# Kernel tuning notes

Measured on AMD Instinct MI355X. Metric: run time of the kernel, lower is better.

Reference implementation:

```python
import jax, jax.numpy as jnp
import numpy as np

EPS = 1e-5

def _ln(x, g, b):
    mu = jnp.mean(x, axis=-1, keepdims=True)
    var = jnp.mean((x - mu) ** 2, axis=-1, keepdims=True)
    return (x - mu) / jnp.sqrt(var + EPS) * g + b

def setup_inputs() -> dict:
    key = jax.random.key(0)
    ks = jax.random.split(key, 8)
    S, B, L, M, D, Nq, H = 4, 256, 256, 4, 512, 4, 2048
    G = (M + 2) * D
    inp = {
        'ns_tokens': jax.random.normal(ks[0], (B, M, D), jnp.float32),
        'seq_tokens': jax.random.normal(ks[1], (S, B, L, D), jnp.float32),
        'seq_padding_masks': jax.random.randint(ks[2], (S, B, L), 0, 2).astype(bool),
        'seq_stats': jax.random.normal(ks[3], (S, B, 6), jnp.float32),
        'gin_gamma': jnp.ones((G,), jnp.float32),
        'gin_beta': jnp.zeros((G,), jnp.float32),
        'stat_W': 0.02 * jax.random.normal(ks[4], (S, 6, D), jnp.float32),
        'stat_b': jnp.zeros((S, D), jnp.float32),
        'stat_ln_g': jnp.ones((S, D), jnp.float32),
        'stat_ln_b': jnp.zeros((S, D), jnp.float32),
        'W1': 0.02 * jax.random.normal(ks[5], (S, Nq, G, H), jnp.float32),
        'b1': jnp.zeros((S, Nq, H), jnp.float32),
        'W2': 0.02 * jax.random.normal(ks[6], (S, Nq, H, D), jnp.float32),
        'b2': jnp.zeros((S, Nq, D), jnp.float32),
        'ln_g': jnp.ones((S, Nq, D), jnp.float32),
        'ln_b': jnp.zeros((S, Nq, D), jnp.float32),
    }
    return inp

def reference(ns_tokens, seq_tokens, seq_padding_masks, seq_stats,
              gin_gamma, gin_beta, stat_W, stat_b, stat_ln_g, stat_ln_b,
              W1, b1, W2, b2, ln_g, ln_b):
    S, B = seq_tokens.shape[0], ns_tokens.shape[0]
    ns_flat = ns_tokens.reshape(B, -1)                       # (B, M*D)
    valid = (~seq_padding_masks).astype(seq_tokens.dtype)[..., None]  # (S,B,L,1)
    denom = jnp.clip(jnp.sum(valid, axis=2), 1.0)            # (S,B,1)
    pooled = jnp.sum(seq_tokens * valid, axis=2) / denom     # (S,B,D)
    stat = jnp.einsum('sbf,sfd->sbd', seq_stats, stat_W) + stat_b[:, None]
    stat = _ln(stat, stat_ln_g[:, None], stat_ln_b[:, None])  # (S,B,D)
    gi = jnp.concatenate([jnp.broadcast_to(ns_flat[None], (S, B, ns_flat.shape[1])), pooled, stat], axis=-1)
    gi = _ln(gi, gin_gamma, gin_beta)                        # (S,B,G)
    h = jax.nn.silu(jnp.einsum('sbg,sqgh->sqbh', gi, W1) + b1[:, :, None])
    q = jnp.einsum('sqbh,sqhd->sqbd', h, W2) + b2[:, :, None]
    q = _ln(q, ln_g[:, :, None], ln_b[:, :, None])           # (S,Nq,B,D)
    return jnp.transpose(q, (0, 2, 1, 3))                    # (S,B,Nq,D)
```

## Files before the change

kernel.cpp:

```cpp
#include <hip/hip_runtime.h>
#include <hip/hip_bf16.h>

#define S_ 4
#define B_ 256
#define L_ 256
#define D_ 512
#define NQ_ 4
#define H_ 2048
#define G_ 3072

typedef __attribute__((ext_vector_type(4))) float f32x4;
typedef __attribute__((ext_vector_type(8))) short s16x8;

__device__ __forceinline__ unsigned short f2bf(float x) {
    __hip_bfloat16 hb = __float2bfloat16(x);
    return reinterpret_cast<unsigned short&>(hb);
}

__device__ __forceinline__ void gll16(const void* g, void* l) {
    __builtin_amdgcn_global_load_lds(
        (const __attribute__((address_space(1))) unsigned int*)g,
        (__attribute__((address_space(3))) unsigned int*)l, 16, 0, 0);
}

__device__ __forceinline__ float block_sum256(float v, float* red) {
    #pragma unroll
    for (int off = 32; off > 0; off >>= 1) v += __shfl_down(v, off, 64);
    int tid = threadIdx.x;
    int lane = tid & 63, wid = tid >> 6;
    if (lane == 0) red[wid] = v;
    __syncthreads();
    float r = (tid < 4) ? red[tid] : 0.f;
    #pragma unroll
    for (int off = 4; off > 0; off >>= 1) r += __shfl_down(r, off, 64);
    if (tid == 0) red[0] = r;
    __syncthreads();
    float out = red[0];
    __syncthreads();
    return out;
}

__global__ __launch_bounds__(256) void poolgi_kernel(
    const float* __restrict__ seq_tokens,
    const unsigned char* __restrict__ masks_raw,
    const float* __restrict__ ns_tokens,
    const float* __restrict__ seq_stats,
    const float* __restrict__ stat_W,
    const float* __restrict__ stat_b,
    const float* __restrict__ stat_ln_g,
    const float* __restrict__ stat_ln_b,
    const float* __restrict__ gin_gamma,
    const float* __restrict__ gin_beta,
    __hip_bfloat16* __restrict__ gi)
{
    const int sb = blockIdx.x;
    const int s = sb >> 8;
    const int b = sb & 255;
    const int tid = threadIdx.x;

    __shared__ float sval[L_];
    __shared__ float scount[4];
    __shared__ f32x4 spart[256];
    __shared__ float spool[D_];
    __shared__ float sstat[D_];
    __shared__ float red[8];
    __shared__ int is_bool_flag;

    if (tid == 0) is_bool_flag = 0;
    __syncthreads();
    {
        unsigned int w = reinterpret_cast<const unsigned int*>(masks_raw)[tid];
        if (w & 0xFFFFFF00u) is_bool_flag = 1;
    }
    __syncthreads();
    const bool is_bool = (is_bool_flag != 0);

    int mval;
    if (is_bool) mval = masks_raw[(size_t)sb * L_ + tid];
    else         mval = reinterpret_cast<const int*>(masks_raw)[(size_t)sb * L_ + tid];
    float valid = mval ? 0.f : 1.f;
    sval[tid] = valid;
    float c = valid;
    #pragma unroll
    for (int off = 32; off > 0; off >>= 1) c += __shfl_down(c, off, 64);
    if ((tid & 63) == 0) scount[tid >> 6] = c;
    __syncthreads();
    const float denom = fmaxf(scount[0] + scount[1] + scount[2] + scount[3], 1.f);

    const float* base = seq_tokens + (size_t)sb * L_ * D_;
    const int cidx = tid & 127;
    const int rg = tid >> 7;
    f32x4 acc = {0.f, 0.f, 0.f, 0.f};
    for (int l = rg; l < L_; l += 2) {
        float vl = sval[l];
        f32x4 v = *reinterpret_cast<const f32x4*>(base + (size_t)l * D_ + cidx * 4);
        acc += v * vl;
    }
    spart[tid] = acc;
    __syncthreads();
    if (tid < 128) {
        f32x4 r = spart[tid] + spart[tid + 128];
        r *= (1.f / denom);
        *reinterpret_cast<f32x4*>(&spool[cidx * 4]) = r;
    }
    __syncthreads();

    float st[6];
    #pragma unroll
    for (int f = 0; f < 6; ++f) st[f] = seq_stats[(size_t)sb * 6 + f];

    float sp[2];
    #pragma unroll
    for (int k = 0; k < 2; ++k) {
        int d = tid + k * 256;
        float a = stat_b[s * D_ + d];
        #pragma unroll
        for (int f = 0; f < 6; ++f) a += st[f] * stat_W[(s * 6 + f) * D_ + d];
        sp[k] = a;
    }
    float ssum = block_sum256(sp[0] + sp[1], red);
    float ssq  = block_sum256(sp[0] * sp[0] + sp[1] * sp[1], red);
    float mu = ssum / D_;
    float var = ssq / D_ - mu * mu;
    float rinv = rsqrtf(var + 1e-5f);
    #pragma unroll
    for (int k = 0; k < 2; ++k) {
        int d = tid + k * 256;
        sstat[d] = (sp[k] - mu) * rinv * stat_ln_g[s * D_ + d] + stat_ln_b[s * D_ + d];
    }
    __syncthreads();

    float gv[12];
    float gsum = 0.f, gsq = 0.f;
    #pragma unroll
    for (int k = 0; k < 12; ++k) {
        int g = tid + k * 256;
        float v;
        if (g < 2048)       v = ns_tokens[(size_t)b * 2048 + g];
        else if (g < 2560)  v = spool[g - 2048];
        else                v = sstat[g - 2560];
        gv[k] = v;
        gsum += v;
        gsq += v * v;
    }
    gsum = block_sum256(gsum, red);
    gsq  = block_sum256(gsq, red);
    mu = gsum / G_;
    var = gsq / G_ - mu * mu;
    rinv = rsqrtf(var + 1e-5f);
    #pragma unroll
    for (int k = 0; k < 12; ++k) {
        int g = tid + k * 256;
        float o = (gv[k] - mu) * rinv * gin_gamma[g] + gin_beta[g];
        gi[(size_t)sb * G_ + g] = __float2bfloat16(o);
    }
}

__global__ __launch_bounds__(256) void gemm1_kernel(
    const __hip_bfloat16* __restrict__ gi,
    const float* __restrict__ W1,
    const float* __restrict__ b1,
    __hip_bfloat16* __restrict__ hbuf)
{
    const int bid = blockIdx.x;
    const int wg = (bid & 7) * 64 + (bid >> 3);
    const int ntile = wg & 31;
    const int sq = wg >> 5;
    const int s = sq >> 2;
    const int tid = threadIdx.x;
    const int lane = tid & 63;
    const int wid = tid >> 6;

    __shared__ __align__(16) unsigned short As[2][256 * 64];
    __shared__ __align__(16) unsigned short Ws[2][64 * 64];

    const __hip_bfloat16* Ab = gi + (size_t)s * B_ * G_;
    const float* Wb = W1 + (size_t)sq * G_ * H_ + ntile * 64;

    f32x4 acc[4][4];
    #pragma unroll
    for (int i = 0; i < 4; ++i)
        #pragma unroll
        for (int j = 0; j < 4; ++j) acc[i][j] = (f32x4){0.f, 0.f, 0.f, 0.f};

    const __hip_bfloat16* aptr[8];
    #pragma unroll
    for (int i = 0; i < 8; ++i) {
        int row = wid * 64 + i * 8 + (lane >> 3);
        int swz = ((lane >> 3) ^ i) & 7;
        aptr[i] = Ab + (size_t)row * G_ + (((lane & 7) ^ swz) * 8);
    }

    const int wn0 = (tid & 15) * 4;
    const int wk0 = (tid >> 4) * 4;
    int offW[4];
    #pragma unroll
    for (int nn = 0; nn < 4; ++nn) {
        int row = wn0 + nn;
        int swz = (row ^ (row >> 3)) & 7;
        offW[nn] = (row * 128 + wk0 * 2) ^ (swz << 4);
    }

    int offA[2][4], offB[2][4];
    #pragma unroll
    for (int kb = 0; kb < 2; ++kb) {
        #pragma unroll
        for (int mi = 0; mi < 4; ++mi) {
            int r = wid * 64 + mi * 16 + (lane & 15);
            int swz = (r ^ (r >> 3)) & 7;
            offA[kb][mi] = r * 128 + ((((lane >> 4) + kb * 4) ^ swz) * 16);
        }
        #pragma unroll
        for (int ni = 0; ni < 4; ++ni) {
            int r = ni * 16 + (lane & 15);
            int swz = (r ^ (r >> 3)) & 7;
            offB[kb][ni] = r * 128 + ((((lane >> 4) + kb * 4) ^ swz) * 16);
        }
    }

    {
        #pragma unroll
        for (int i = 0; i < 8; ++i)
            gll16(aptr[i], &As[0][(wid * 64 + i * 8) * 64]);
        const float* wp = Wb + (size_t)wk0 * H_ + wn0;
        f32x4 w0[4];
        #pragma unroll
        for (int kk = 0; kk < 4; ++kk)
            w0[kk] = *reinterpret_cast<const f32x4*>(wp + (size_t)kk * H_);
        #pragma unroll
        for (int nn = 0; nn < 4; ++nn) {
            unsigned long long pk =
                (unsigned long long)f2bf(w0[0][nn]) |
                ((unsigned long long)f2bf(w0[1][nn]) << 16) |
                ((unsigned long long)f2bf(w0[2][nn]) << 32) |
                ((unsigned long long)f2bf(w0[3][nn]) << 48);
            *reinterpret_cast<unsigned long long*>(reinterpret_cast<char*>(&Ws[0][0]) + offW[nn]) = pk;
        }
        __syncthreads();
    }

    for (int kt = 0; kt < G_ / 64; ++kt) {
        const int cur = kt & 1, nxt = cur ^ 1;
        const bool pf = (kt < G_ / 64 - 1);
        f32x4 wv[4];
        if (pf) {
            const int kb2 = (kt + 1) * 64;
            #pragma unroll
            for (int i = 0; i < 8; ++i)
                gll16(aptr[i] + kb2, &As[nxt][(wid * 64 + i * 8) * 64]);
            const float* wp = Wb + (size_t)(kb2 + wk0) * H_ + wn0;
            #pragma unroll
            for (int kk = 0; kk < 4; ++kk)
                wv[kk] = *reinterpret_cast<const f32x4*>(wp + (size_t)kk * H_);
        }

        const char* Al = reinterpret_cast<const char*>(&As[cur][0]);
        const char* Wl = reinterpret_cast<const char*>(&Ws[cur][0]);
        #pragma unroll
        for (int kb = 0; kb < 2; ++kb) {
            s16x8 af[4], bfr[4];
            #pragma unroll
            for (int mi = 0; mi < 4; ++mi)
                af[mi] = *reinterpret_cast<const s16x8*>(Al + offA[kb][mi]);
            #pragma unroll
            for (int ni = 0; ni < 4; ++ni)
                bfr[ni] = *reinterpret_cast<const s16x8*>(Wl + offB[kb][ni]);
            #pragma unroll
            for (int mi = 0; mi < 4; ++mi)
                #pragma unroll
                for (int ni = 0; ni < 4; ++ni)
                    acc[mi][ni] = __builtin_amdgcn_mfma_f32_16x16x32_bf16(af[mi], bfr[ni], acc[mi][ni], 0, 0, 0);
        }

        if (pf) {
            #pragma unroll
            for (int nn = 0; nn < 4; ++nn) {
                unsigned long long pk =
                    (unsigned long long)f2bf(wv[0][nn]) |
                    ((unsigned long long)f2bf(wv[1][nn]) << 16) |
                    ((unsigned long long)f2bf(wv[2][nn]) << 32) |
                    ((unsigned long long)f2bf(wv[3][nn]) << 48);
                *reinterpret_cast<unsigned long long*>(reinterpret_cast<char*>(&Ws[nxt][0]) + offW[nn]) = pk;
            }
        }
        __syncthreads();
    }

    const float* b1p = b1 + (size_t)sq * H_ + ntile * 64;
    __hip_bfloat16* hp = hbuf + (size_t)sq * B_ * H_;
    #pragma unroll
    for (int mi = 0; mi < 4; ++mi)
        #pragma unroll
        for (int ni = 0; ni < 4; ++ni)
            #pragma unroll
            for (int r = 0; r < 4; ++r) {
                int row = wid * 64 + mi * 16 + ((lane >> 4) << 2) + r;
                int coll = ni * 16 + (lane & 15);
                float x = acc[mi][ni][r] + b1p[coll];
                float sg = 1.f / (1.f + __expf(-x));
                hp[(size_t)row * H_ + ntile * 64 + coll] = __float2bfloat16(x * sg);
            }
}

__global__ __launch_bounds__(256) void gemm2_kernel(
    const __hip_bfloat16* __restrict__ hbuf,
    const float* __restrict__ W2,
    float* __restrict__ qpre)
{
    const int ntile = blockIdx.x;
    const int mtile = blockIdx.y;
    const int sq = blockIdx.z;
    const int tid = threadIdx.x;
    const int lane = tid & 63;
    const int wid = tid >> 6;
    const int wm = wid >> 1, wn = wid & 1;

    __shared__ __align__(16) unsigned short As[128 * 64];
    __shared__ __align__(16) unsigned short Ws[64 * 64];

    const __hip_bfloat16* Ab = hbuf + ((size_t)sq * B_ + mtile * 128) * H_;
    const float* Wb = W2 + (size_t)sq * H_ * D_ + ntile * 64;

    f32x4 acc[4][2];
    #pragma unroll
    for (int i = 0; i < 4; ++i)
        #pragma unroll
        for (int j = 0; j < 2; ++j) acc[i][j] = (f32x4){0.f, 0.f, 0.f, 0.f};

    const int wn0 = (tid & 15) * 4;
    const int wk0 = (tid >> 4) * 4;

    for (int kt = 0; kt < H_ / 64; ++kt) {
        const int kbase = kt * 64;
        __syncthreads();
        #pragma unroll
        for (int i = 0; i < 4; ++i) {
            int slot = i * 256 + tid;
            int row = slot >> 3, cc = slot & 7;
            int swz = (row ^ (row >> 3)) & 7;
            s16x8 v = *reinterpret_cast<const s16x8*>(Ab + (size_t)row * H_ + kbase + cc * 8);
            *reinterpret_cast<s16x8*>(&As[row * 64 + ((cc ^ swz) * 8)]) = v;
        }
        float wv[4][4];
        #pragma unroll
        for (int kk = 0; kk < 4; ++kk) {
            f32x4 t = *reinterpret_cast<const f32x4*>(Wb + (size_t)(kbase + wk0 + kk) * D_ + wn0);
            #pragma unroll
            for (int j = 0; j < 4; ++j) wv[kk][j] = t[j];
        }
        #pragma unroll
        for (int nn = 0; nn < 4; ++nn) {
            int row = wn0 + nn;
            int swz = (row ^ (row >> 3)) & 7;
            unsigned long long pk =
                (unsigned long long)f2bf(wv[0][nn]) |
                ((unsigned long long)f2bf(wv[1][nn]) << 16) |
                ((unsigned long long)f2bf(wv[2][nn]) << 32) |
                ((unsigned long long)f2bf(wv[3][nn]) << 48);
            int byteoff = (row * 128 + wk0 * 2) ^ (swz << 4);
            *reinterpret_cast<unsigned long long*>(reinterpret_cast<char*>(Ws) + byteoff) = pk;
        }
        __syncthreads();
        #pragma unroll
        for (int kb = 0; kb < 2; ++kb) {
            s16x8 af[4], bfr[2];
            #pragma unroll
            for (int mi = 0; mi < 4; ++mi) {
                int r = wm * 64 + mi * 16 + (lane & 15);
                int swz = (r ^ (r >> 3)) & 7;
                int chunk = ((lane >> 4) + kb * 4) ^ swz;
                af[mi] = *reinterpret_cast<const s16x8*>(&As[r * 64 + chunk * 8]);
            }
            #pragma unroll
            for (int ni = 0; ni < 2; ++ni) {
                int r = wn * 32 + ni * 16 + (lane & 15);
                int swz = (r ^ (r >> 3)) & 7;
                int chunk = ((lane >> 4) + kb * 4) ^ swz;
                bfr[ni] = *reinterpret_cast<const s16x8*>(&Ws[r * 64 + chunk * 8]);
            }
            #pragma unroll
            for (int mi = 0; mi < 4; ++mi)
                #pragma unroll
                for (int ni = 0; ni < 2; ++ni)
                    acc[mi][ni] = __builtin_amdgcn_mfma_f32_16x16x32_bf16(af[mi], bfr[ni], acc[mi][ni], 0, 0, 0);
        }
    }
    #pragma unroll
    for (int mi = 0; mi < 4; ++mi)
        #pragma unroll
        for (int ni = 0; ni < 2; ++ni)
            #pragma unroll
            for (int r = 0; r < 4; ++r) {
                int row = mtile * 128 + wm * 64 + mi * 16 + ((lane >> 4) << 2) + r;
                int col = ntile * 64 + wn * 32 + ni * 16 + (lane & 15);
                qpre[((size_t)sq * B_ + row) * D_ + col] = acc[mi][ni][r];
            }
}

__global__ __launch_bounds__(256) void lnout_kernel(
    const float* __restrict__ qpre,
    const float* __restrict__ b2,
    const float* __restrict__ lng,
    const float* __restrict__ lnb,
    float* __restrict__ out)
{
    const int idx = blockIdx.x;
    const int sq = idx >> 8;
    const int b = idx & 255;
    const int tid = threadIdx.x;
    __shared__ float red[8];

    float v[2];
    #pragma unroll
    for (int k = 0; k < 2; ++k) {
        int d = tid + k * 256;
        v[k] = qpre[(size_t)idx * D_ + d] + b2[sq * D_ + d];
    }
    float sum = block_sum256(v[0] + v[1], red);
    float sq2 = block_sum256(v[0] * v[0] + v[1] * v[1], red);
    float mu = sum / D_;
    float var = sq2 / D_ - mu * mu;
    float rinv = rsqrtf(var + 1e-5f);
    const int s = sq >> 2, q = sq & 3;
    #pragma unroll
    for (int k = 0; k < 2; ++k) {
        int d = tid + k * 256;
        float o = (v[k] - mu) * rinv * lng[sq * D_ + d] + lnb[sq * D_ + d];
        out[(((size_t)s * B_ + b) * NQ_ + q) * D_ + d] = o;
    }
}

extern "C" void kernel_launch(void* const* d_in, const int* in_sizes, int n_in,
                              void* d_out, int out_size, void* d_ws, size_t ws_size,
                              hipStream_t stream) {
    const float* ns_tokens   = (const float*)d_in[0];
    const float* seq_tokens  = (const float*)d_in[1];
    const unsigned char* masks = (const unsigned char*)d_in[2];
    const float* seq_stats   = (const float*)d_in[3];
    const float* gin_gamma   = (const float*)d_in[4];
    const float* gin_beta    = (const float*)d_in[5];
    const float* stat_W      = (const float*)d_in[6];
    const float* stat_b      = (const float*)d_in[7];
    const float* stat_ln_g   = (const float*)d_in[8];
    const float* stat_ln_b   = (const float*)d_in[9];
    const float* W1          = (const float*)d_in[10];
    const float* b1          = (const float*)d_in[11];
    const float* W2          = (const float*)d_in[12];
    const float* b2          = (const float*)d_in[13];
    const float* ln_g        = (const float*)d_in[14];
    const float* ln_b        = (const float*)d_in[15];
    float* out = (float*)d_out;

    char* ws = (char*)d_ws;
    __hip_bfloat16* gi   = (__hip_bfloat16*)(ws);
    __hip_bfloat16* hbuf = (__hip_bfloat16*)(ws + 6291456);
    float* qpre          = (float*)(ws + 6291456 + 16777216);

    poolgi_kernel<<<dim3(S_ * B_), dim3(256), 0, stream>>>(
        seq_tokens, masks, ns_tokens, seq_stats, stat_W, stat_b,
        stat_ln_g, stat_ln_b, gin_gamma, gin_beta, gi);
    gemm1_kernel<<<dim3(32 * S_ * NQ_), dim3(256), 0, stream>>>(gi, W1, b1, hbuf);
    gemm2_kernel<<<dim3(D_ / 64, B_ / 128, S_ * NQ_), dim3(256), 0, stream>>>(hbuf, W2, qpre);
    lnout_kernel<<<dim3(S_ * NQ_ * B_), dim3(256), 0, stream>>>(qpre, b2, ln_g, ln_b, out);
}
```

Before: 288.7 us.

## Split pooling kernel, refine gemm1 pipeline waits, remap gemm2 blocks, bf16 qpre

Splits the fused pool+gi kernel into a pure pooling kernel and a separate gi/LayerNorm kernel, so the memory-bound pooling pass has less shared-memory and register pressure. In gemm1, the prefetch is made unconditional with a clamped index and uses 32-bit offsets, and the full __syncthreads is replaced by explicit vmcnt/lgkmcnt waits plus s_barrier so global loads stay in flight across the MFMA loop. gemm2 gets a 1D grid with an XCD-aware block remap, issues its W loads before the A loads, and writes its intermediate in bf16 instead of fp32. This adds one kernel launch and an extra pooled buffer round trip, and the bf16 intermediate loses some precision before the final LayerNorm.

```diff
diff --git a/kernel.cpp b/kernel.cpp
--- a/kernel.cpp
+++ b/kernel.cpp
@@ -40,9 +40,58 @@
     return out;
 }
 
-__global__ __launch_bounds__(256) void poolgi_kernel(
+__global__ __launch_bounds__(256) void pool_kernel(
     const float* __restrict__ seq_tokens,
     const unsigned char* __restrict__ masks_raw,
+    float* __restrict__ pooled)
+{
+    const int sb = blockIdx.x;
+    const int tid = threadIdx.x;
+    __shared__ float sval[L_];
+    __shared__ float scount[4];
+    __shared__ f32x4 spart[256];
+    __shared__ int is_bool_flag;
+
+    if (tid == 0) is_bool_flag = 0;
+    __syncthreads();
+    {
+        unsigned int w = reinterpret_cast<const unsigned int*>(masks_raw)[tid];
+        if (w & 0xFFFFFF00u) is_bool_flag = 1;
+    }
+    __syncthreads();
+    const bool is_bool = (is_bool_flag != 0);
+
+    int mval;
+    if (is_bool) mval = masks_raw[(size_t)sb * L_ + tid];
+    else         mval = reinterpret_cast<const int*>(masks_raw)[(size_t)sb * L_ + tid];
+    float valid = mval ? 0.f : 1.f;
+    sval[tid] = valid;
+    float c = valid;
+    #pragma unroll
+    for (int off = 32; off > 0; off >>= 1) c += __shfl_down(c, off, 64);
+    if ((tid & 63) == 0) scount[tid >> 6] = c;
+    __syncthreads();
+    const float denom = fmaxf(scount[0] + scount[1] + scount[2] + scount[3], 1.f);
+
+    const float* base = seq_tokens + (size_t)sb * L_ * D_;
+    const int cidx = tid & 127;
+    const int rg = tid >> 7;
+    f32x4 acc = {0.f, 0.f, 0.f, 0.f};
+    for (int l = rg; l < L_; l += 2) {
+        float vl = sval[l];
+        f32x4 v = *reinterpret_cast<const f32x4*>(base + (size_t)l * D_ + cidx * 4);
+        acc += v * vl;
+    }
+    spart[tid] = acc;
+    __syncthreads();
+    if (tid < 128) {
+        f32x4 r = spart[tid] + spart[tid + 128];
+        r *= (1.f / denom);
+        *reinterpret_cast<f32x4*>(pooled + (size_t)sb * D_ + cidx * 4) = r;
+    }
+}
+
+__global__ __launch_bounds__(256) void gi_kernel(
     const float* __restrict__ ns_tokens,
     const float* __restrict__ seq_stats,
     const float* __restrict__ stat_W,
@@ -51,59 +100,15 @@
     const float* __restrict__ stat_ln_b,
     const float* __restrict__ gin_gamma,
     const float* __restrict__ gin_beta,
+    const float* __restrict__ pooled,
     __hip_bfloat16* __restrict__ gi)
 {
     const int sb = blockIdx.x;
     const int s = sb >> 8;
     const int b = sb & 255;
     const int tid = threadIdx.x;
-
-    __shared__ float sval[L_];
-    __shared__ float scount[4];
-    __shared__ f32x4 spart[256];
-    __shared__ float spool[D_];
+    __shared__ float red[8];
     __shared__ float sstat[D_];
-    __shared__ float red[8];
-    __shared__ int is_bool_flag;
-
-    if (tid == 0) is_bool_flag = 0;
-    __syncthreads();
-    {
-        unsigned int w = reinterpret_cast<const unsigned int*>(masks_raw)[tid];
-        if (w & 0xFFFFFF00u) is_bool_flag = 1;
-    }
-    __syncthreads();
-    const bool is_bool = (is_bool_flag != 0);
-
-    int mval;
-    if (is_bool) mval = masks_raw[(size_t)sb * L_ + tid];
-    else         mval = reinterpret_cast<const int*>(masks_raw)[(size_t)sb * L_ + tid];
-    float valid = mval ? 0.f : 1.f;
-    sval[tid] = valid;
-    float c = valid;
-    #pragma unroll
-    for (int off = 32; off > 0; off >>= 1) c += __shfl_down(c, off, 64);
-    if ((tid & 63) == 0) scount[tid >> 6] = c;
-    __syncthreads();
-    const float denom = fmaxf(scount[0] + scount[1] + scount[2] + scount[3], 1.f);
-
-    const float* base = seq_tokens + (size_t)sb * L_ * D_;
-    const int cidx = tid & 127;
-    const int rg = tid >> 7;
-    f32x4 acc = {0.f, 0.f, 0.f, 0.f};
-    for (int l = rg; l < L_; l += 2) {
-        float vl = sval[l];
-        f32x4 v = *reinterpret_cast<const f32x4*>(base + (size_t)l * D_ + cidx * 4);
-        acc += v * vl;
-    }
-    spart[tid] = acc;
-    __syncthreads();
-    if (tid < 128) {
-        f32x4 r = spart[tid] + spart[tid + 128];
-        r *= (1.f / denom);
-        *reinterpret_cast<f32x4*>(&spool[cidx * 4]) = r;
-    }
-    __syncthreads();
 
     float st[6];
     #pragma unroll
@@ -137,7 +142,7 @@
         int g = tid + k * 256;
         float v;
         if (g < 2048)       v = ns_tokens[(size_t)b * 2048 + g];
-        else if (g < 2560)  v = spool[g - 2048];
+        else if (g < 2560)  v = pooled[(size_t)sb * D_ + (g - 2048)];
         else                v = sstat[g - 2560];
         gv[k] = v;
         gsum += v;
@@ -174,7 +179,7 @@
     __shared__ __align__(16) unsigned short As[2][256 * 64];
     __shared__ __align__(16) unsigned short Ws[2][64 * 64];
 
-    const __hip_bfloat16* Ab = gi + (size_t)s * B_ * G_;
+    const char* Ag = reinterpret_cast<const char*>(gi + (size_t)s * B_ * G_);
     const float* Wb = W1 + (size_t)sq * G_ * H_ + ntile * 64;
 
     f32x4 acc[4][4];
@@ -183,25 +188,25 @@
         #pragma unroll
         for (int j = 0; j < 4; ++j) acc[i][j] = (f32x4){0.f, 0.f, 0.f, 0.f};
 
-    const __hip_bfloat16* aptr[8];
+    unsigned aoff[8];
     #pragma unroll
     for (int i = 0; i < 8; ++i) {
         int row = wid * 64 + i * 8 + (lane >> 3);
         int swz = ((lane >> 3) ^ i) & 7;
-        aptr[i] = Ab + (size_t)row * G_ + (((lane & 7) ^ swz) * 8);
+        aoff[i] = (unsigned)row * (G_ * 2) + (((lane & 7) ^ swz) * 16);
     }
 
     const int wn0 = (tid & 15) * 4;
     const int wk0 = (tid >> 4) * 4;
-    int offW[4];
+    unsigned offW[4];
     #pragma unroll
     for (int nn = 0; nn < 4; ++nn) {
         int row = wn0 + nn;
         int swz = (row ^ (row >> 3)) & 7;
-        offW[nn] = (row * 128 + wk0 * 2) ^ (swz << 4);
-    }
-
-    int offA[2][4], offB[2][4];
+        offW[nn] = (unsigned)((row * 128 + wk0 * 2) ^ (swz << 4));
+    }
+
+    unsigned offA[2][4], offB[2][4];
     #pragma unroll
     for (int kb = 0; kb < 2; ++kb) {
         #pragma unroll
@@ -219,14 +224,14 @@
     }
 
     {
+        char* dst = reinterpret_cast<char*>(&As[0][0]);
         #pragma unroll
         for (int i = 0; i < 8; ++i)
-            gll16(aptr[i], &As[0][(wid * 64 + i * 8) * 64]);
-        const float* wp = Wb + (size_t)wk0 * H_ + wn0;
+            gll16(Ag + aoff[i], dst + (wid * 64 + i * 8) * 128);
         f32x4 w0[4];
         #pragma unroll
         for (int kk = 0; kk < 4; ++kk)
-            w0[kk] = *reinterpret_cast<const f32x4*>(wp + (size_t)kk * H_);
+            w0[kk] = *reinterpret_cast<const f32x4*>(Wb + (size_t)(wk0 + kk) * H_ + wn0);
         #pragma unroll
         for (int nn = 0; nn < 4; ++nn) {
             unsigned long long pk =
@@ -236,23 +241,30 @@
                 ((unsigned long long)f2bf(w0[3][nn]) << 48);
             *reinterpret_cast<unsigned long long*>(reinterpret_cast<char*>(&Ws[0][0]) + offW[nn]) = pk;
         }
-        __syncthreads();
+        asm volatile("s_waitcnt lgkmcnt(0)" ::: "memory");
+        __builtin_amdgcn_s_barrier();
     }
 
     for (int kt = 0; kt < G_ / 64; ++kt) {
         const int cur = kt & 1, nxt = cur ^ 1;
-        const bool pf = (kt < G_ / 64 - 1);
-        f32x4 wv[4];
-        if (pf) {
-            const int kb2 = (kt + 1) * 64;
+        const int kn = (kt < G_ / 64 - 1) ? kt + 1 : G_ / 64 - 1;
+
+        f32x4 wreg[4];
+        {
+            const float* wp = Wb + (size_t)(kn * 64 + wk0) * H_ + wn0;
+            #pragma unroll
+            for (int kk = 0; kk < 4; ++kk)
+                wreg[kk] = *reinterpret_cast<const f32x4*>(wp + (size_t)kk * H_);
+        }
+        {
+            char* dst = reinterpret_cast<char*>(&As[nxt][0]);
+            const unsigned kbyte = (unsigned)kn * 128;
             #pragma unroll
             for (int i = 0; i < 8; ++i)
-                gll16(aptr[i] + kb2, &As[nxt][(wid * 64 + i * 8) * 64]);
-            const float* wp = Wb + (size_t)(kb2 + wk0) * H_ + wn0;
-            #pragma unroll
-            for (int kk = 0; kk < 4; ++kk)
-                wv[kk] = *reinterpret_cast<const f32x4*>(wp + (size_t)kk * H_);
-        }
+                gll16(Ag + (aoff[i] + kbyte), dst + (wid * 64 + i * 8) * 128);
+        }
+        asm volatile("s_waitcnt vmcnt(12)" ::: "memory");
+        __builtin_amdgcn_sched_barrier(0);
 
         const char* Al = reinterpret_cast<const char*>(&As[cur][0]);
         const char* Wl = reinterpret_cast<const char*>(&Ws[cur][0]);
@@ -272,18 +284,17 @@
                     acc[mi][ni] = __builtin_amdgcn_mfma_f32_16x16x32_bf16(af[mi], bfr[ni], acc[mi][ni], 0, 0, 0);
         }
 
-        if (pf) {
-            #pragma unroll
-            for (int nn = 0; nn < 4; ++nn) {
-                unsigned long long pk =
-                    (unsigned long long)f2bf(wv[0][nn]) |
-                    ((unsigned long long)f2bf(wv[1][nn]) << 16) |
-                    ((unsigned long long)f2bf(wv[2][nn]) << 32) |
-                    ((unsigned long long)f2bf(wv[3][nn]) << 48);
-                *reinterpret_cast<unsigned long long*>(reinterpret_cast<char*>(&Ws[nxt][0]) + offW[nn]) = pk;
-            }
-        }
-        __syncthreads();
+        #pragma unroll
+        for (int nn = 0; nn < 4; ++nn) {
+            unsigned long long pk =
+                (unsigned long long)f2bf(wreg[0][nn]) |
+                ((unsigned long long)f2bf(wreg[1][nn]) << 16) |
+                ((unsigned long long)f2bf(wreg[2][nn]) << 32) |
+                ((unsigned long long)f2bf(wreg[3][nn]) << 48);
+            *reinterpret_cast<unsigned long long*>(reinterpret_cast<char*>(&Ws[nxt][0]) + offW[nn]) = pk;
+        }
+        asm volatile("s_waitcnt lgkmcnt(0)" ::: "memory");
+        __builtin_amdgcn_s_barrier();
     }
 
     const float* b1p = b1 + (size_t)sq * H_ + ntile * 64;
@@ -305,11 +316,13 @@
 __global__ __launch_bounds__(256) void gemm2_kernel(
     const __hip_bfloat16* __restrict__ hbuf,
     const float* __restrict__ W2,
-    float* __restrict__ qpre)
+    __hip_bfloat16* __restrict__ qpre)
 {
-    const int ntile = blockIdx.x;
-    const int mtile = blockIdx.y;
-    const int sq = blockIdx.z;
+    const int bid = blockIdx.x;
+    const int wg = (bid & 7) * 32 + (bid >> 3);
+    const int ntile = wg & 7;
+    const int mtile = (wg >> 3) & 1;
+    const int sq = wg >> 4;
     const int tid = threadIdx.x;
     const int lane = tid & 63;
     const int wid = tid >> 6;
@@ -333,6 +346,13 @@
     for (int kt = 0; kt < H_ / 64; ++kt) {
         const int kbase = kt * 64;
         __syncthreads();
+        float wv[4][4];
+        #pragma unroll
+        for (int kk = 0; kk < 4; ++kk) {
+            f32x4 t = *reinterpret_cast<const f32x4*>(Wb + (size_t)(kbase + wk0 + kk) * D_ + wn0);
+            #pragma unroll
+            for (int j = 0; j < 4; ++j) wv[kk][j] = t[j];
+        }
         #pragma unroll
         for (int i = 0; i < 4; ++i) {
             int slot = i * 256 + tid;
@@ -340,13 +360,6 @@
             int swz = (row ^ (row >> 3)) & 7;
             s16x8 v = *reinterpret_cast<const s16x8*>(Ab + (size_t)row * H_ + kbase + cc * 8);
             *reinterpret_cast<s16x8*>(&As[row * 64 + ((cc ^ swz) * 8)]) = v;
-        }
-        float wv[4][4];
-        #pragma unroll
-        for (int kk = 0; kk < 4; ++kk) {
-            f32x4 t = *reinterpret_cast<const f32x4*>(Wb + (size_t)(kbase + wk0 + kk) * D_ + wn0);
-            #pragma unroll
-            for (int j = 0; j < 4; ++j) wv[kk][j] = t[j];
         }
         #pragma unroll
         for (int nn = 0; nn < 4; ++nn) {
@@ -393,12 +406,12 @@
             for (int r = 0; r < 4; ++r) {
                 int row = mtile * 128 + wm * 64 + mi * 16 + ((lane >> 4) << 2) + r;
                 int col = ntile * 64 + wn * 32 + ni * 16 + (lane & 15);
-                qpre[((size_t)sq * B_ + row) * D_ + col] = acc[mi][ni][r];
+                qpre[((size_t)sq * B_ + row) * D_ + col] = __float2bfloat16(acc[mi][ni][r]);
             }
 }
 
 __global__ __launch_bounds__(256) void lnout_kernel(
-    const float* __restrict__ qpre,
+    const __hip_bfloat16* __restrict__ qpre,
     const float* __restrict__ b2,
     const float* __restrict__ lng,
     const float* __restrict__ lnb,
@@ -414,7 +427,7 @@
     #pragma unroll
     for (int k = 0; k < 2; ++k) {
         int d = tid + k * 256;
-        v[k] = qpre[(size_t)idx * D_ + d] + b2[sq * D_ + d];
+        v[k] = __bfloat162float(qpre[(size_t)idx * D_ + d]) + b2[sq * D_ + d];
     }
     float sum = block_sum256(v[0] + v[1], red);
     float sq2 = block_sum256(v[0] * v[0] + v[1] * v[1], red);
@@ -452,14 +465,16 @@
     float* out = (float*)d_out;
 
     char* ws = (char*)d_ws;
-    __hip_bfloat16* gi   = (__hip_bfloat16*)(ws);
-    __hip_bfloat16* hbuf = (__hip_bfloat16*)(ws + 6291456);
-    float* qpre          = (float*)(ws + 6291456 + 16777216);
-
-    poolgi_kernel<<<dim3(S_ * B_), dim3(256), 0, stream>>>(
-        seq_tokens, masks, ns_tokens, seq_stats, stat_W, stat_b,
-        stat_ln_g, stat_ln_b, gin_gamma, gin_beta, gi);
+    float* pooled        = (float*)(ws);
+    __hip_bfloat16* gi   = (__hip_bfloat16*)(ws + 2097152);
+    __hip_bfloat16* hbuf = (__hip_bfloat16*)(ws + 2097152 + 6291456);
+    __hip_bfloat16* qpre = (__hip_bfloat16*)(ws + 2097152 + 6291456 + 16777216);
+
+    pool_kernel<<<dim3(S_ * B_), dim3(256), 0, stream>>>(seq_tokens, masks, pooled);
+    gi_kernel<<<dim3(S_ * B_), dim3(256), 0, stream>>>(ns_tokens, seq_stats, stat_W, stat_b,
+                                                       stat_ln_g, stat_ln_b, gin_gamma, gin_beta,
+                                                       pooled, gi);
     gemm1_kernel<<<dim3(32 * S_ * NQ_), dim3(256), 0, stream>>>(gi, W1, b1, hbuf);
-    gemm2_kernel<<<dim3(D_ / 64, B_ / 128, S_ * NQ_), dim3(256), 0, stream>>>(hbuf, W2, qpre);
+    gemm2_kernel<<<dim3(2 * D_ / 64 * S_ * NQ_), dim3(256), 0, stream>>>(hbuf, W2, qpre);
     lnout_kernel<<<dim3(S_ * NQ_ * B_), dim3(256), 0, stream>>>(qpre, b2, ln_g, ln_b, out);
 }
```

Result: faster. 268.8 us (-6.9%).
